# Performance work log

Hardware: AMD Instinct MI355X
Metric: run time of the kernel (lower is better)

## Reference

```python
import jax, jax.numpy as jnp
import numpy as np

INITIAL_RADIUS = 1.0  # init_kwargs: initial_radius > 0 -> distance-softmax branch


def reference(xyz, sparse_xyz, sparse_flow, resol_factor, K):
    # xyz: [B,3,N], sparse_xyz: [B,3,M], sparse_flow: [B,3,M]
    q = jnp.transpose(xyz, (0, 2, 1))            # [B,N,3]
    p = jnp.transpose(sparse_xyz, (0, 2, 1))     # [B,M,3]
    flow = jnp.transpose(sparse_flow, (0, 2, 1))  # [B,M,3]

    sigma = INITIAL_RADIUS * resol_factor
    qs = q / sigma
    ps = p / sigma

    # pairwise Euclidean distances [B,N,M]
    sq = (jnp.sum(qs * qs, -1)[:, :, None]
          + jnp.sum(ps * ps, -1)[:, None, :]
          - 2.0 * jnp.einsum('bnc,bmc->bnm', qs, ps))
    dist = jnp.sqrt(jnp.maximum(sq, 1e-12))

    # K nearest: smallest distances
    neg_d, idx = jax.lax.top_k(-dist, K)          # [B,N,K]
    K_dist = -neg_d                               # [B,N,K]

    # gather flow of the K neighbors: [B,N,K,3]
    grouped_flow = jnp.take_along_axis(flow[:, None, :, :], idx[..., None], axis=2)

    # softmax over -distance along K, weighted sum
    K_w = jax.nn.softmax(-K_dist, axis=2)         # [B,N,K]
    dense_flow = jnp.sum(K_w[..., None] * grouped_flow, axis=2)  # [B,N,3]

    return jnp.transpose(dense_flow, (0, 2, 1))   # [B,3,N]


def setup_inputs() -> dict:
    key = jax.random.key(0)
    k1, k2, k3 = jax.random.split(key, 3)
    B, N, M = 4, 16384, 4096
    return {
        'xyz': jax.random.normal(k1, (B, 3, N), dtype=jnp.float32),
        'sparse_xyz': jax.random.normal(k2, (B, 3, M), dtype=jnp.float32),
        'sparse_flow': jax.random.normal(k3, (B, 3, M), dtype=jnp.float32),
        'resol_factor': 1,
        'K': 5,
    }
```

## Files before the change

kernel.cpp:

```cpp
#include <hip/hip_runtime.h>
#include <math.h>
#include <stdint.h>


#define KNN 5
#define GRID 8
#define NCELL (GRID * GRID * GRID)
#define SPAN_TH 64
#define SLICES 8
#define BLOCK (SLICES * 64)
#define EPSM 1e-3f

typedef unsigned int u32;

__device__ __forceinline__ float get_inv_sigma(const int* __restrict__ rf) {
    const int ri = rf[0];
    const float sigma = (ri >= 1 && ri <= 1000000) ? (float)ri : __int_as_float(ri);
    return 1.0f / sigma;
}

__device__ __forceinline__ float rfl_f(float v) {
    return __int_as_float(__builtin_amdgcn_readfirstlane(__float_as_int(v)));
}

__device__ __forceinline__ int cid1(float x, float lo, float ich) {
    const int c = (int)floorf((x - lo) * ich);
    return c < 0 ? 0 : (c > GRID - 1 ? GRID - 1 : c);
}

__device__ __forceinline__ int sp3(int v) {
    return (v & 1) | ((v & 2) << 2) | ((v & 4) << 4);
}

__device__ __forceinline__ u32 fenc(float f) {
    const u32 b = __float_as_uint(f);
    return (b & 0x80000000u) ? ~b : (b | 0x80000000u);
}
__device__ __forceinline__ float fdec(u32 u) {
    return __uint_as_float((u & 0x80000000u) ? (u & 0x7FFFFFFFu) : ~u);
}

__device__ __forceinline__ void bb_load(const u32* __restrict__ minU,
                                        const u32* __restrict__ maxU, int b,
                                        float& lox, float& loy, float& loz,
                                        float& chx, float& chy, float& chz) {
    const float sc = (1.0f / GRID) * (1.0f + 4e-6f);
    const float Lx = fdec(minU[b * 3 + 0]);
    const float Ly = fdec(minU[b * 3 + 1]);
    const float Lz = fdec(minU[b * 3 + 2]);
    lox = Lx; loy = Ly; loz = Lz;
    chx = (fdec(maxU[b * 3 + 0]) - Lx) * sc + 1e-30f;
    chy = (fdec(maxU[b * 3 + 1]) - Ly) * sc + 1e-30f;
    chz = (fdec(maxU[b * 3 + 2]) - Lz) * sc + 1e-30f;
}

#define CE_FULL(k, ki, c, ci)                          \
    {                                                  \
        const bool sw = (c) < (k);                     \
        const float vmn = fminf(k, c);                 \
        const float vmx = fmaxf(k, c);                 \
        const u32 nki = sw ? (ci) : (ki);              \
        const u32 nci = sw ? (ki) : (ci);              \
        (k) = vmn; (c) = vmx; (ki) = nki; (ci) = nci;  \
    }
#define CE_LAST(k, ki, c, ci)                          \
    {                                                  \
        const bool sw = (c) < (k);                     \
        (ki) = sw ? (ci) : (ki);                       \
        (k) = fminf(k, c);                             \
    }

#define LAD(P, CI)                                     \
    {                                                  \
        float t_ = qx * (P).x;                         \
        t_ = fmaf(qy, (P).y, t_);                      \
        t_ = fmaf(qz, (P).z, t_);                      \
        float c_ = fmaf(-2.0f, t_, (P).w);             \
        u32 ci_ = (u32)(CI);                           \
        CE_FULL(e0, i0, c_, ci_)                       \
        CE_FULL(e1, i1, c_, ci_)                       \
        CE_FULL(e2, i2, c_, ci_)                       \
        CE_FULL(e3, i3, c_, ci_)                       \
        CE_LAST(e4, i4, c_, ci_)                       \
    }


__global__ __launch_bounds__(256)
void prep_kernel(const float* __restrict__ sxyz, const int* __restrict__ rf,
                 float4* __restrict__ pts, int M, int total) {
    const int t = blockIdx.x * 256 + threadIdx.x;
    if (t >= total) return;
    const float inv = get_inv_sigma(rf);
    const int b = t / M, m = t - b * M;
    const float* sb = sxyz + (size_t)b * 3 * M;
    const float x = sb[m] * inv;
    const float y = sb[M + m] * inv;
    const float z = sb[2 * M + m] * inv;
    pts[t] = make_float4(x, y, z, fmaf(x, x, fmaf(y, y, z * z)));
}

template <bool USE_PTS>
__global__ __launch_bounds__(BLOCK, 8)
void knn_kernel(const float* __restrict__ xyz,
                const float* __restrict__ sxyz,
                const float* __restrict__ sflow,
                const int* __restrict__ rf,
                const float4* __restrict__ pts,
                float* __restrict__ out,
                int N, int M) {
    __shared__ float sval_d[SLICES * KNN * 64];
    __shared__ u32   sval_i[SLICES * KNN * 64];

    const int tid  = threadIdx.x;
    const int lane = tid & 63;
    const int wid  = tid >> 6;
    const int swid = __builtin_amdgcn_readfirstlane(wid);
    const int gpb  = N / 64;
    const int b    = blockIdx.x / gpb;
    const int grp  = blockIdx.x - b * gpb;
    const int n    = grp * 64 + lane;

    const float inv = get_inv_sigma(rf);
    const float* qb = xyz + (size_t)b * 3 * N;
    const float qx = qb[n] * inv;
    const float qy = qb[N + n] * inv;
    const float qz = qb[2 * N + n] * inv;
    const float qq = fmaf(qx, qx, fmaf(qy, qy, qz * qz));

    const int CH = M / SLICES;
    const int j0 = swid * CH;

    float e0 = 1e30f, e1 = 1e30f, e2 = 1e30f, e3 = 1e30f, e4 = 1e30f;
    u32   i0 = 0, i1 = 0, i2 = 0, i3 = 0, i4 = 0;

    if constexpr (USE_PTS) {
        const float4* __restrict__ P = pts + (size_t)b * M + j0;
#pragma unroll 4
        for (int j = 0; j < CH; ++j) {
            const float4 p = P[j];
            LAD(p, j0 + j)
        }
    } else {
        const float* __restrict__ sb = sxyz + (size_t)b * 3 * M;
#pragma unroll 4
        for (int j = 0; j < CH; ++j) {
            const float px = sb[j0 + j] * inv;
            const float py = sb[M + j0 + j] * inv;
            const float pz = sb[2 * M + j0 + j] * inv;
            const float pw = fmaf(px, px, fmaf(py, py, pz * pz));
            const float4 p = make_float4(px, py, pz, pw);
            LAD(p, j0 + j)
        }
    }

    sval_d[(wid * KNN + 0) * 64 + lane] = e0;  sval_i[(wid * KNN + 0) * 64 + lane] = i0;
    sval_d[(wid * KNN + 1) * 64 + lane] = e1;  sval_i[(wid * KNN + 1) * 64 + lane] = i1;
    sval_d[(wid * KNN + 2) * 64 + lane] = e2;  sval_i[(wid * KNN + 2) * 64 + lane] = i2;
    sval_d[(wid * KNN + 3) * 64 + lane] = e3;  sval_i[(wid * KNN + 3) * 64 + lane] = i3;
    sval_d[(wid * KNN + 4) * 64 + lane] = e4;  sval_i[(wid * KNN + 4) * 64 + lane] = i4;
    __syncthreads();

    if (wid == 0) {
        float m0 = 1e30f, m1 = 1e30f, m2 = 1e30f, m3 = 1e30f, m4 = 1e30f;
        u32   g0 = 0, g1 = 0, g2 = 0, g3 = 0, g4 = 0;
#pragma unroll
        for (int w = 0; w < SLICES; ++w) {
#pragma unroll
            for (int k = 0; k < KNN; ++k) {
                float c = sval_d[(w * KNN + k) * 64 + lane];
                u32  ci = sval_i[(w * KNN + k) * 64 + lane];
                CE_FULL(m0, g0, c, ci)
                CE_FULL(m1, g1, c, ci)
                CE_FULL(m2, g2, c, ci)
                CE_FULL(m3, g3, c, ci)
                CE_LAST(m4, g4, c, ci)
            }
        }

        const float d0 = sqrtf(fmaxf(m0 + qq, 1e-12f));
        const float d1 = sqrtf(fmaxf(m1 + qq, 1e-12f));
        const float d2 = sqrtf(fmaxf(m2 + qq, 1e-12f));
        const float d3 = sqrtf(fmaxf(m3 + qq, 1e-12f));
        const float d4 = sqrtf(fmaxf(m4 + qq, 1e-12f));
        const float w0 = 1.0f;
        const float w1 = expf(d0 - d1);
        const float w2 = expf(d0 - d2);
        const float w3 = expf(d0 - d3);
        const float w4 = expf(d0 - d4);
        const float inv_wsum = 1.0f / (w0 + w1 + w2 + w3 + w4);

        const float* fb = sflow + (size_t)b * 3 * M;
        float ax = 0.f, ay = 0.f, az = 0.f;
        ax = fmaf(w0, fb[g0], ax); ay = fmaf(w0, fb[M + g0], ay); az = fmaf(w0, fb[2 * M + g0], az);
        ax = fmaf(w1, fb[g1], ax); ay = fmaf(w1, fb[M + g1], ay); az = fmaf(w1, fb[2 * M + g1], az);
        ax = fmaf(w2, fb[g2], ax); ay = fmaf(w2, fb[M + g2], ay); az = fmaf(w2, fb[2 * M + g2], az);
        ax = fmaf(w3, fb[g3], ax); ay = fmaf(w3, fb[M + g3], ay); az = fmaf(w3, fb[2 * M + g3], az);
        ax = fmaf(w4, fb[g4], ax); ay = fmaf(w4, fb[M + g4], ay); az = fmaf(w4, fb[2 * M + g4], az);

        float* ob = out + (size_t)b * 3 * N;
        ob[n]         = ax * inv_wsum;
        ob[N + n]     = ay * inv_wsum;
        ob[2 * N + n] = az * inv_wsum;
    }
}


__global__ __launch_bounds__(256)
void bbox_atomic_kernel(const float* __restrict__ sxyz, const int* __restrict__ rf,
                        u32* __restrict__ minU, u32* __restrict__ maxU, int M) {
    const int per = M / 256;
    const int b = blockIdx.x / per;
    const int m = (blockIdx.x - b * per) * 256 + threadIdx.x;
    const float inv = get_inv_sigma(rf);
    const float* sb = sxyz + (size_t)b * 3 * M;
    const float x = sb[m] * inv, y = sb[M + m] * inv, z = sb[2 * M + m] * inv;
    float lx = x, ly = y, lz = z, hx = x, hy = y, hz = z;
#pragma unroll
    for (int mm = 1; mm < 64; mm <<= 1) {
        lx = fminf(lx, __shfl_xor(lx, mm, 64));
        ly = fminf(ly, __shfl_xor(ly, mm, 64));
        lz = fminf(lz, __shfl_xor(lz, mm, 64));
        hx = fmaxf(hx, __shfl_xor(hx, mm, 64));
        hy = fmaxf(hy, __shfl_xor(hy, mm, 64));
        hz = fmaxf(hz, __shfl_xor(hz, mm, 64));
    }
    if ((threadIdx.x & 63) == 0) {
        atomicMin(&minU[b * 3 + 0], fenc(lx));
        atomicMin(&minU[b * 3 + 1], fenc(ly));
        atomicMin(&minU[b * 3 + 2], fenc(lz));
        atomicMax(&maxU[b * 3 + 0], fenc(hx));
        atomicMax(&maxU[b * 3 + 1], fenc(hy));
        atomicMax(&maxU[b * 3 + 2], fenc(hz));
    }
}

__global__ __launch_bounds__(256)
void hist_kernel2(const float* __restrict__ xyz, const float* __restrict__ sxyz,
                  const int* __restrict__ rf, const u32* __restrict__ minU,
                  const u32* __restrict__ maxU, int* __restrict__ histAll,
                  int N, int M, int B) {
    const int t = blockIdx.x * 256 + threadIdx.x;
    const int TC = B * M;
    const float inv = get_inv_sigma(rf);
    float x, y, z; int b, slice;
    if (t < TC) {
        b = t / M; const int i = t - b * M;
        const float* sb = sxyz + (size_t)b * 3 * M;
        x = sb[i] * inv; y = sb[M + i] * inv; z = sb[2 * M + i] * inv;
        slice = b;
    } else if (t < TC + B * N) {
        const int t2 = t - TC;
        b = t2 / N; const int i = t2 - b * N;
        const float* qb = xyz + (size_t)b * 3 * N;
        x = qb[i] * inv; y = qb[N + i] * inv; z = qb[2 * N + i] * inv;
        slice = B + b;
    } else return;
    float lox, loy, loz, chx, chy, chz;
    bb_load(minU, maxU, b, lox, loy, loz, chx, chy, chz);
    const int cell = (sp3(cid1(x, lox, 1.0f / chx)) << 2) |
                     (sp3(cid1(y, loy, 1.0f / chy)) << 1) |
                      sp3(cid1(z, loz, 1.0f / chz));
    atomicAdd(&histAll[(size_t)slice * NCELL + cell], 1);
}

__global__ __launch_bounds__(NCELL)
void scan_kernel2(const int* __restrict__ histAll, int2* __restrict__ off2C,
                  int* __restrict__ curAll, int B) {
    __shared__ int sc[NCELL];
    const int s = blockIdx.x;
    const int t = threadIdx.x;
    const int h = histAll[(size_t)s * NCELL + t];
    sc[t] = h;
    __syncthreads();
    for (int d = 1; d < NCELL; d <<= 1) {
        const int v = (t >= d) ? sc[t - d] : 0;
        __syncthreads();
        sc[t] += v;
        __syncthreads();
    }
    const int excl = sc[t] - h;
    curAll[(size_t)s * NCELL + t] = excl;
    if (s < B) off2C[(size_t)s * NCELL + t] = make_int2(excl, excl + h);
}

__global__ __launch_bounds__(256)
void scatter_kernel2(const float* __restrict__ xyz, const float* __restrict__ sxyz,
                     const int* __restrict__ rf, const u32* __restrict__ minU,
                     const u32* __restrict__ maxU, int* __restrict__ curAll,
                     float4* __restrict__ ptsS, float4* __restrict__ qS,
                     int* __restrict__ idxS, int N, int M, int B) {
    const int t = blockIdx.x * 256 + threadIdx.x;
    const int TC = B * M;
    const float inv = get_inv_sigma(rf);
    float x, y, z; int b, i, slice;
    bool isQ;
    if (t < TC) {
        b = t / M; i = t - b * M;
        const float* sb = sxyz + (size_t)b * 3 * M;
        x = sb[i] * inv; y = sb[M + i] * inv; z = sb[2 * M + i] * inv;
        slice = b; isQ = false;
    } else if (t < TC + B * N) {
        const int t2 = t - TC;
        b = t2 / N; i = t2 - b * N;
        const float* qb = xyz + (size_t)b * 3 * N;
        x = qb[i] * inv; y = qb[N + i] * inv; z = qb[2 * N + i] * inv;
        slice = B + b; isQ = true;
    } else return;
    float lox, loy, loz, chx, chy, chz;
    bb_load(minU, maxU, b, lox, loy, loz, chx, chy, chz);
    const int cell = (sp3(cid1(x, lox, 1.0f / chx)) << 2) |
                     (sp3(cid1(y, loy, 1.0f / chy)) << 1) |
                      sp3(cid1(z, loz, 1.0f / chz));
    const int slot = atomicAdd(&curAll[(size_t)slice * NCELL + cell], 1);
    if (isQ) {
        qS[(size_t)b * N + slot] = make_float4(x, y, z, __int_as_float(i));
    } else {
        ptsS[(size_t)b * M + slot] = make_float4(x, y, z, fmaf(x, x, fmaf(y, y, z * z)));
        idxS[(size_t)b * M + slot] = i;
    }
}


#define CELLP(CZ)                                                               \
    {                                                                           \
        const float glz_ = fmaf((float)(CZ), chz, loz);                         \
        const float cqz_ = fminf(fmaxf(qz, glz_), glz_ + chz);                  \
        const float dzl_ = qz - cqz_;                                           \
        const float d3_ = fmaf(dzl_, dzl_, dxy2);                               \
        const float cmp_ = fmaf(e4 + qq, 1.00001f, EPSM);                       \
        if (!__all(d3_ > cmp_)) {                                               \
            const int cell_ = mxy | sp3(CZ);                                    \
            const int2 oo_ = off2b[cell_];                                      \
            const int base_ = __builtin_amdgcn_readfirstlane(oo_.x);            \
            const int end_ = __builtin_amdgcn_readfirstlane(oo_.y);             \
            int j_ = base_;                                                     \
            for (; j_ + 4 <= end_; j_ += 4) {                                   \
                const float4 p0_ = Pb[j_];                                      \
                const float4 p1_ = Pb[j_ + 1];                                  \
                const float4 p2_ = Pb[j_ + 2];                                  \
                const float4 p3_ = Pb[j_ + 3];                                  \
                LAD(p0_, j_) LAD(p1_, j_ + 1)                                   \
                LAD(p2_, j_ + 2) LAD(p3_, j_ + 3)                               \
            }                                                                   \
            for (; j_ < end_; ++j_) {                                           \
                const float4 pp_ = Pb[j_];                                      \
                LAD(pp_, j_)                                                    \
            }                                                                   \
        }                                                                       \
    }

__global__ __launch_bounds__(BLOCK, 8)
void knn_grid8_kernel(const float4* __restrict__ qS, const float4* __restrict__ ptsS,
                      const int* __restrict__ idxS, const int2* __restrict__ off2C,
                      const u32* __restrict__ minU, const u32* __restrict__ maxU,
                      const float* __restrict__ sflow,
                      float* __restrict__ out, int N, int M) {
    __shared__ float sval_d[SLICES * KNN * 64];
    __shared__ u32   sval_i[SLICES * KNN * 64];
    __shared__ float se4[SLICES * 64];

    const int tid  = threadIdx.x;
    const int lane = tid & 63;
    const int wid  = tid >> 6;
    const int swid = __builtin_amdgcn_readfirstlane(wid);
    const int gpb  = N >> 6;
    const int b    = blockIdx.x / gpb;
    const int grp  = blockIdx.x - b * gpb;

    const float4 q4 = qS[(size_t)b * N + grp * 64 + lane];
    const float qx = q4.x, qy = q4.y, qz = q4.z;
    const int n = __float_as_int(q4.w);
    const float qq = fmaf(qx, qx, fmaf(qy, qy, qz * qz));

    float wlx = qx, wly = qy, wlz = qz, whx = qx, why = qy, whz = qz;
#pragma unroll
    for (int m = 1; m < 64; m <<= 1) {
        wlx = fminf(wlx, __shfl_xor(wlx, m, 64));
        whx = fmaxf(whx, __shfl_xor(whx, m, 64));
        wly = fminf(wly, __shfl_xor(wly, m, 64));
        why = fmaxf(why, __shfl_xor(why, m, 64));
        wlz = fminf(wlz, __shfl_xor(wlz, m, 64));
        whz = fmaxf(whz, __shfl_xor(whz, m, 64));
    }
    wlx = rfl_f(wlx) - EPSM; whx = rfl_f(whx) + EPSM;
    wly = rfl_f(wly) - EPSM; why = rfl_f(why) + EPSM;
    wlz = rfl_f(wlz) - EPSM; whz = rfl_f(whz) + EPSM;

    float lox, loy, loz, chx, chy, chz;
    bb_load(minU, maxU, b, lox, loy, loz, chx, chy, chz);
    const float hmin = fminf(chx, fminf(chy, chz));

    const int clx = cid1(wlx, lox, 1.0f / chx), cxh = cid1(whx, lox, 1.0f / chx);
    const int cly = cid1(wly, loy, 1.0f / chy), cyh = cid1(why, loy, 1.0f / chy);
    const int clz = cid1(wlz, loz, 1.0f / chz), czh = cid1(whz, loz, 1.0f / chz);

    float e0 = 1e30f, e1 = 1e30f, e2 = 1e30f, e3 = 1e30f, e4 = 1e30f;
    u32   i0 = 0, i1 = 0, i2 = 0, i3 = 0, i4 = 0;

    const float4* __restrict__ Pb = ptsS + (size_t)b * M;
    const int2* __restrict__ off2b = off2C + (size_t)b * NCELL;

    const int span = (cxh - clx + 1) * (cyh - cly + 1) * (czh - clz + 1);
    if (span > SPAN_TH) {
        const int CH = M / SLICES;
        const int j0 = swid * CH;
        const float4* __restrict__ P = Pb + j0;
#pragma unroll 4
        for (int j = 0; j < CH; ++j) {
            const float4 p = P[j];
            LAD(p, j0 + j)
        }
    } else {
        int ctr = 0;
        for (int cx = clx; cx <= cxh; ++cx) {
            const float glx = fmaf((float)cx, chx, lox);
            const float cqx = fminf(fmaxf(qx, glx), glx + chx);
            const float dxl = qx - cqx;
            const float dxx = dxl * dxl;
            const int mx = sp3(cx) << 2;
            for (int cy = cly; cy <= cyh; ++cy) {
                const float gly = fmaf((float)cy, chy, loy);
                const float cqy = fminf(fmaxf(qy, gly), gly + chy);
                const float dyl = qy - cqy;
                const float dxy2 = fmaf(dyl, dyl, dxx);
                const int mxy = mx | (sp3(cy) << 1);
                for (int cz = clz; cz <= czh; ++cz) {
                    if (((ctr++) & 7) == wid) { CELLP(cz) }
                }
            }
        }
        se4[wid * 64 + lane] = e4;
        __syncthreads();
        float bnd = se4[lane];
#pragma unroll
        for (int w = 1; w < SLICES; ++w) bnd = fminf(bnd, se4[w * 64 + lane]);
        bnd += qq;
#pragma unroll
        for (int mm = 1; mm < 64; mm <<= 1) bnd = fmaxf(bnd, __shfl_xor(bnd, mm, 64));
        float TwR = rfl_f(bnd);

        for (int r = 1; r <= GRID; ++r) {
            float own = e4 + qq;
#pragma unroll
            for (int mm = 1; mm < 64; mm <<= 1) own = fmaxf(own, __shfl_xor(own, mm, 64));
            TwR = fminf(TwR, rfl_f(own));
            if (r >= 2) {
                const float bd = (float)(r - 1) * hmin - EPSM;
                if (bd > 0.0f && bd * bd > fmaf(TwR, 1.00001f, EPSM)) break;
            }
            const int x0 = clx - r < 0 ? 0 : clx - r;
            const int x1 = cxh + r > GRID - 1 ? GRID - 1 : cxh + r;
            const int y0 = cly - r < 0 ? 0 : cly - r;
            const int y1 = cyh + r > GRID - 1 ? GRID - 1 : cyh + r;
            const int z0 = clz - r < 0 ? 0 : clz - r;
            const int z1 = czh + r > GRID - 1 ? GRID - 1 : czh + r;
            for (int cx = x0; cx <= x1; ++cx) {
                const int rx = cx < clx ? clx - cx : (cx > cxh ? cx - cxh : 0);
                const float glx = fmaf((float)cx, chx, lox);
                const float cqx = fminf(fmaxf(qx, glx), glx + chx);
                const float dxl = qx - cqx;
                const float dxx = dxl * dxl;
                const int mx = sp3(cx) << 2;
                for (int cy = y0; cy <= y1; ++cy) {
                    const int ry = cy < cly ? cly - cy : (cy > cyh ? cy - cyh : 0);
                    if (((ctr++) & 7) == wid) {
                        const float gly = fmaf((float)cy, chy, loy);
                        const float cqy = fminf(fmaxf(qy, gly), gly + chy);
                        const float dyl = qy - cqy;
                        const float dxy2 = fmaf(dyl, dyl, dxx);
                        const float cmpc = fmaf(e4 + qq, 1.00001f, EPSM);
                        if (!__all(dxy2 > cmpc)) {
                            const int mxy = mx | (sp3(cy) << 1);
                            if ((rx > ry ? rx : ry) == r) {
                                for (int cz = z0; cz <= z1; ++cz) { CELLP(cz) }
                            } else {
                                if (clz - r >= 0) { CELLP(clz - r) }
                                if (czh + r <= GRID - 1) { CELLP(czh + r) }
                            }
                        }
                    }
                }
            }
        }
    }

    sval_d[(wid * KNN + 0) * 64 + lane] = e0;  sval_i[(wid * KNN + 0) * 64 + lane] = i0;
    sval_d[(wid * KNN + 1) * 64 + lane] = e1;  sval_i[(wid * KNN + 1) * 64 + lane] = i1;
    sval_d[(wid * KNN + 2) * 64 + lane] = e2;  sval_i[(wid * KNN + 2) * 64 + lane] = i2;
    sval_d[(wid * KNN + 3) * 64 + lane] = e3;  sval_i[(wid * KNN + 3) * 64 + lane] = i3;
    sval_d[(wid * KNN + 4) * 64 + lane] = e4;  sval_i[(wid * KNN + 4) * 64 + lane] = i4;
    __syncthreads();

    if (wid == 0) {
        float m0 = 1e30f, m1 = 1e30f, m2 = 1e30f, m3 = 1e30f, m4 = 1e30f;
        u32 g0 = 0, g1 = 0, g2 = 0, g3 = 0, g4 = 0;
#pragma unroll
        for (int w = 0; w < SLICES; ++w) {
#pragma unroll
            for (int k = 0; k < KNN; ++k) {
                float c = sval_d[(w * KNN + k) * 64 + lane];
                u32 ci = sval_i[(w * KNN + k) * 64 + lane];
                CE_FULL(m0, g0, c, ci)
                CE_FULL(m1, g1, c, ci)
                CE_FULL(m2, g2, c, ci)
                CE_FULL(m3, g3, c, ci)
                CE_LAST(m4, g4, c, ci)
            }
        }

        const float d0 = sqrtf(fmaxf(m0 + qq, 1e-12f));
        const float d1 = sqrtf(fmaxf(m1 + qq, 1e-12f));
        const float d2 = sqrtf(fmaxf(m2 + qq, 1e-12f));
        const float d3 = sqrtf(fmaxf(m3 + qq, 1e-12f));
        const float d4 = sqrtf(fmaxf(m4 + qq, 1e-12f));
        const float w0 = 1.0f;
        const float w1 = expf(d0 - d1);
        const float w2 = expf(d0 - d2);
        const float w3 = expf(d0 - d3);
        const float w4 = expf(d0 - d4);
        const float inv_wsum = 1.0f / (w0 + w1 + w2 + w3 + w4);

        const int* __restrict__ idxb = idxS + (size_t)b * M;
        const int o0 = idxb[g0], o1 = idxb[g1], o2 = idxb[g2], o3 = idxb[g3], o4 = idxb[g4];
        const float* fb = sflow + (size_t)b * 3 * M;
        float ax = 0.f, ay = 0.f, az = 0.f;
        ax = fmaf(w0, fb[o0], ax); ay = fmaf(w0, fb[M + o0], ay); az = fmaf(w0, fb[2 * M + o0], az);
        ax = fmaf(w1, fb[o1], ax); ay = fmaf(w1, fb[M + o1], ay); az = fmaf(w1, fb[2 * M + o1], az);
        ax = fmaf(w2, fb[o2], ax); ay = fmaf(w2, fb[M + o2], ay); az = fmaf(w2, fb[2 * M + o2], az);
        ax = fmaf(w3, fb[o3], ax); ay = fmaf(w3, fb[M + o3], ay); az = fmaf(w3, fb[2 * M + o3], az);
        ax = fmaf(w4, fb[o4], ax); ay = fmaf(w4, fb[M + o4], ay); az = fmaf(w4, fb[2 * M + o4], az);

        float* ob = out + (size_t)b * 3 * N;
        ob[n]         = ax * inv_wsum;
        ob[N + n]     = ay * inv_wsum;
        ob[2 * N + n] = az * inv_wsum;
    }
}

extern "C" void kernel_launch(void* const* d_in, const int* in_sizes, int n_in,
                              void* d_out, int out_size, void* d_ws, size_t ws_size,
                              hipStream_t stream) {
    const float* xyz   = (const float*)d_in[0];
    const float* sxyz  = (const float*)d_in[1];
    const float* sflow = (const float*)d_in[2];
    const int*   rf    = (const int*)d_in[3];

    const int B = 4;
    const int N = in_sizes[0] / (3 * B);
    const int M = in_sizes[1] / (3 * B);
    float* out = (float*)d_out;

    size_t o = 0;
    float4* ptsS  = (float4*)((char*)d_ws + o); o += (size_t)B * M * sizeof(float4);
    float4* qS    = (float4*)((char*)d_ws + o); o += (size_t)B * N * sizeof(float4);
    int*   idxS   = (int*)((char*)d_ws + o);    o += (size_t)B * M * 4;
    u32*   minU   = (u32*)((char*)d_ws + o);    o += (size_t)B * 3 * 4;
    u32*   maxU   = (u32*)((char*)d_ws + o);    o += (size_t)B * 3 * 4;
    int*   histAll= (int*)((char*)d_ws + o);    o += (size_t)2 * B * NCELL * 4;
    int*   curAll = (int*)((char*)d_ws + o);    o += (size_t)2 * B * NCELL * 4;
    int2*  off2C  = (int2*)((char*)d_ws + o);   o += (size_t)B * NCELL * 8;
    const size_t need = o;

    if (ws_size >= need && (N % 64) == 0 && (M % 256) == 0) {
        const int total = B * (M + N);
        hipMemsetAsync(minU, 0xFF, (size_t)B * 3 * 4, stream);
        hipMemsetAsync(maxU, 0x00, (size_t)B * 3 * 4 + (size_t)2 * B * NCELL * 4, stream);
        bbox_atomic_kernel<<<dim3(B * (M / 256)), dim3(256), 0, stream>>>(
            sxyz, rf, minU, maxU, M);
        hist_kernel2<<<dim3((total + 255) / 256), dim3(256), 0, stream>>>(
            xyz, sxyz, rf, minU, maxU, histAll, N, M, B);
        scan_kernel2<<<dim3(2 * B), dim3(NCELL), 0, stream>>>(
            histAll, off2C, curAll, B);
        scatter_kernel2<<<dim3((total + 255) / 256), dim3(256), 0, stream>>>(
            xyz, sxyz, rf, minU, maxU, curAll, ptsS, qS, idxS, N, M, B);
        knn_grid8_kernel<<<dim3(B * (N / 64)), dim3(BLOCK), 0, stream>>>(
            qS, ptsS, idxS, off2C, minU, maxU, sflow, out, N, M);
    } else {
        const dim3 grid(B * (N / 64));
        const dim3 block(BLOCK);
        const size_t needOld = (size_t)B * M * sizeof(float4);
        if (ws_size >= needOld) {
            float4* pts = (float4*)d_ws;
            prep_kernel<<<dim3((B * M + 255) / 256), dim3(256), 0, stream>>>(
                sxyz, rf, pts, M, B * M);
            knn_kernel<true><<<grid, block, 0, stream>>>(xyz, sxyz, sflow, rf, pts, out, N, M);
        } else {
            knn_kernel<false><<<grid, block, 0, stream>>>(xyz, sxyz, sflow, rf, nullptr, out, N, M);
        }
    }
}
```

Before: 269.5 us.

## Seed KNN bound from home cell and prune wide-span queries by cell

Each query first scans its own grid cell and takes the fifth-best distance there as an upper bound. That bound tightens the cell-pruning test from the start and replaces the shared-memory, block-wide bound reduction along with its __syncthreads. The wide-span path no longer brute-forces all M points: it walks all grid cells outward from the centre and skips cells that cannot hold a closer neighbour. The bbox minimum is now stored negated and updated with atomicMax, so a single memset clears all the counters. The cost is an extra serial scan of the home cell per query, and more divergence when the home cell is crowded.

```diff
diff --git a/kernel.cpp b/kernel.cpp
--- a/kernel.cpp
+++ b/kernel.cpp
@@ -45,9 +45,9 @@
                                         float& lox, float& loy, float& loz,
                                         float& chx, float& chy, float& chz) {
     const float sc = (1.0f / GRID) * (1.0f + 4e-6f);
-    const float Lx = fdec(minU[b * 3 + 0]);
-    const float Ly = fdec(minU[b * 3 + 1]);
-    const float Lz = fdec(minU[b * 3 + 2]);
+    const float Lx = -fdec(minU[b * 3 + 0]);
+    const float Ly = -fdec(minU[b * 3 + 1]);
+    const float Lz = -fdec(minU[b * 3 + 2]);
     lox = Lx; loy = Ly; loz = Lz;
     chx = (fdec(maxU[b * 3 + 0]) - Lx) * sc + 1e-30f;
     chy = (fdec(maxU[b * 3 + 1]) - Ly) * sc + 1e-30f;
@@ -225,9 +225,9 @@
         hz = fmaxf(hz, __shfl_xor(hz, mm, 64));
     }
     if ((threadIdx.x & 63) == 0) {
-        atomicMin(&minU[b * 3 + 0], fenc(lx));
-        atomicMin(&minU[b * 3 + 1], fenc(ly));
-        atomicMin(&minU[b * 3 + 2], fenc(lz));
+        atomicMax(&minU[b * 3 + 0], fenc(-lx));
+        atomicMax(&minU[b * 3 + 1], fenc(-ly));
+        atomicMax(&minU[b * 3 + 2], fenc(-lz));
         atomicMax(&maxU[b * 3 + 0], fenc(hx));
         atomicMax(&maxU[b * 3 + 1], fenc(hy));
         atomicMax(&maxU[b * 3 + 2], fenc(hz));
@@ -321,31 +321,35 @@
 }
 
 
+#define CELLSCAN(CELLIDX)                                                       \
+    {                                                                           \
+        const int2 oo_ = off2b[CELLIDX];                                        \
+        const int base_ = __builtin_amdgcn_readfirstlane(oo_.x);                \
+        const int end_ = __builtin_amdgcn_readfirstlane(oo_.y);                 \
+        int j_ = base_;                                                         \
+        for (; j_ + 4 <= end_; j_ += 4) {                                       \
+            const float4 p0_ = Pb[j_];                                          \
+            const float4 p1_ = Pb[j_ + 1];                                      \
+            const float4 p2_ = Pb[j_ + 2];                                      \
+            const float4 p3_ = Pb[j_ + 3];                                      \
+            LAD(p0_, j_) LAD(p1_, j_ + 1)                                       \
+            LAD(p2_, j_ + 2) LAD(p3_, j_ + 3)                                   \
+        }                                                                       \
+        for (; j_ < end_; ++j_) {                                               \
+            const float4 pp_ = Pb[j_];                                          \
+            LAD(pp_, j_)                                                        \
+        }                                                                       \
+    }
+
 #define CELLP(CZ)                                                               \
     {                                                                           \
         const float glz_ = fmaf((float)(CZ), chz, loz);                         \
         const float cqz_ = fminf(fmaxf(qz, glz_), glz_ + chz);                  \
         const float dzl_ = qz - cqz_;                                           \
         const float d3_ = fmaf(dzl_, dzl_, dxy2);                               \
-        const float cmp_ = fmaf(e4 + qq, 1.00001f, EPSM);                       \
+        const float cmp_ = fmaf(fminf(e4, bw) + qq, 1.00001f, EPSM);            \
         if (!__all(d3_ > cmp_)) {                                               \
-            const int cell_ = mxy | sp3(CZ);                                    \
-            const int2 oo_ = off2b[cell_];                                      \
-            const int base_ = __builtin_amdgcn_readfirstlane(oo_.x);            \
-            const int end_ = __builtin_amdgcn_readfirstlane(oo_.y);             \
-            int j_ = base_;                                                     \
-            for (; j_ + 4 <= end_; j_ += 4) {                                   \
-                const float4 p0_ = Pb[j_];                                      \
-                const float4 p1_ = Pb[j_ + 1];                                  \
-                const float4 p2_ = Pb[j_ + 2];                                  \
-                const float4 p3_ = Pb[j_ + 3];                                  \
-                LAD(p0_, j_) LAD(p1_, j_ + 1)                                   \
-                LAD(p2_, j_ + 2) LAD(p3_, j_ + 3)                               \
-            }                                                                   \
-            for (; j_ < end_; ++j_) {                                           \
-                const float4 pp_ = Pb[j_];                                      \
-                LAD(pp_, j_)                                                    \
-            }                                                                   \
+            CELLSCAN(mxy | sp3(CZ))                                             \
         }                                                                       \
     }
 
@@ -357,12 +361,10 @@
                       float* __restrict__ out, int N, int M) {
     __shared__ float sval_d[SLICES * KNN * 64];
     __shared__ u32   sval_i[SLICES * KNN * 64];
-    __shared__ float se4[SLICES * 64];
 
     const int tid  = threadIdx.x;
     const int lane = tid & 63;
     const int wid  = tid >> 6;
-    const int swid = __builtin_amdgcn_readfirstlane(wid);
     const int gpb  = N >> 6;
     const int b    = blockIdx.x / gpb;
     const int grp  = blockIdx.x - b * gpb;
@@ -400,15 +402,49 @@
     const float4* __restrict__ Pb = ptsS + (size_t)b * M;
     const int2* __restrict__ off2b = off2C + (size_t)b * NCELL;
 
+    float bw;
+    {
+        const int hcell = (sp3(cid1(qx, lox, 1.0f / chx)) << 2) |
+                          (sp3(cid1(qy, loy, 1.0f / chy)) << 1) |
+                           sp3(cid1(qz, loz, 1.0f / chz));
+        const int2 ho = off2b[hcell];
+        float v0 = 1e30f, v1 = 1e30f, v2 = 1e30f, v3 = 1e30f, v4 = 1e30f;
+        for (int j = ho.x; j < ho.y; ++j) {
+            const float4 p = Pb[j];
+            float t = qx * p.x;
+            t = fmaf(qy, p.y, t);
+            t = fmaf(qz, p.z, t);
+            float c = fmaf(-2.0f, t, p.w);
+            float mn;
+            mn = fminf(v0, c); c = fmaxf(v0, c); v0 = mn;
+            mn = fminf(v1, c); c = fmaxf(v1, c); v1 = mn;
+            mn = fminf(v2, c); c = fmaxf(v2, c); v2 = mn;
+            mn = fminf(v3, c); c = fmaxf(v3, c); v3 = mn;
+            v4 = fminf(v4, c);
+        }
+        bw = v4;
+    }
+
     const int span = (cxh - clx + 1) * (cyh - cly + 1) * (czh - clz + 1);
     if (span > SPAN_TH) {
-        const int CH = M / SLICES;
-        const int j0 = swid * CH;
-        const float4* __restrict__ P = Pb + j0;
-#pragma unroll 4
-        for (int j = 0; j < CH; ++j) {
-            const float4 p = P[j];
-            LAD(p, j0 + j)
+        const int ccx = (clx + cxh) >> 1, ccy = (cly + cyh) >> 1, ccz = (clz + czh) >> 1;
+        const int c0 = (sp3(ccx) << 2) | (sp3(ccy) << 1) | sp3(ccz);
+        for (int k = wid; k < NCELL; k += SLICES) {
+            const int c = (c0 + k) & (NCELL - 1);
+            const int cx = ((c >> 2) & 1) | ((c >> 4) & 2) | ((c >> 6) & 4);
+            const int cy = ((c >> 1) & 1) | ((c >> 3) & 2) | ((c >> 5) & 4);
+            const int cz = (c & 1) | ((c >> 2) & 2) | ((c >> 4) & 4);
+            const float glx = fmaf((float)cx, chx, lox);
+            const float gly = fmaf((float)cy, chy, loy);
+            const float glz = fmaf((float)cz, chz, loz);
+            const float dxl = qx - fminf(fmaxf(qx, glx), glx + chx);
+            const float dyl = qy - fminf(fmaxf(qy, gly), gly + chy);
+            const float dzl = qz - fminf(fmaxf(qz, glz), glz + chz);
+            const float d3 = fmaf(dzl, dzl, fmaf(dyl, dyl, dxl * dxl));
+            const float cmp = fmaf(fminf(e4, bw) + qq, 1.00001f, EPSM);
+            if (!__all(d3 > cmp)) {
+                CELLSCAN(c)
+            }
         }
     } else {
         int ctr = 0;
@@ -429,18 +465,9 @@
                 }
             }
         }
-        se4[wid * 64 + lane] = e4;
-        __syncthreads();
-        float bnd = se4[lane];
-#pragma unroll
-        for (int w = 1; w < SLICES; ++w) bnd = fminf(bnd, se4[w * 64 + lane]);
-        bnd += qq;
-#pragma unroll
-        for (int mm = 1; mm < 64; mm <<= 1) bnd = fmaxf(bnd, __shfl_xor(bnd, mm, 64));
-        float TwR = rfl_f(bnd);
-
+        float TwR = 1e30f;
         for (int r = 1; r <= GRID; ++r) {
-            float own = e4 + qq;
+            float own = fminf(e4, bw) + qq;
 #pragma unroll
             for (int mm = 1; mm < 64; mm <<= 1) own = fmaxf(own, __shfl_xor(own, mm, 64));
             TwR = fminf(TwR, rfl_f(own));
@@ -468,7 +495,7 @@
                         const float cqy = fminf(fmaxf(qy, gly), gly + chy);
                         const float dyl = qy - cqy;
                         const float dxy2 = fmaf(dyl, dyl, dxx);
-                        const float cmpc = fmaf(e4 + qq, 1.00001f, EPSM);
+                        const float cmpc = fmaf(fminf(e4, bw) + qq, 1.00001f, EPSM);
                         if (!__all(dxy2 > cmpc)) {
                             const int mxy = mx | (sp3(cy) << 1);
                             if ((rx > ry ? rx : ry) == r) {
@@ -563,8 +590,8 @@
 
     if (ws_size >= need && (N % 64) == 0 && (M % 256) == 0) {
         const int total = B * (M + N);
-        hipMemsetAsync(minU, 0xFF, (size_t)B * 3 * 4, stream);
-        hipMemsetAsync(maxU, 0x00, (size_t)B * 3 * 4 + (size_t)2 * B * NCELL * 4, stream);
+        hipMemsetAsync(minU, 0x00,
+                       (size_t)B * 3 * 4 * 2 + (size_t)2 * B * NCELL * 4, stream);
         bbox_atomic_kernel<<<dim3(B * (M / 256)), dim3(256), 0, stream>>>(
             sxyz, rf, minU, maxU, M);
         hist_kernel2<<<dim3((total + 255) / 256), dim3(256), 0, stream>>>(
```

After: 279.3 us. +3.6%, slower.
